# Performance work log

Measured on AMD Instinct MI355X. Metric: run time of the kernel, lower is better.

Reference implementation:

```python
import jax, jax.numpy as jnp
import numpy as np

NEG_SLOPE = 0.2


def gat_conv(x, src, dst, W, a_src, a_dst, bias, concat):
    # x: [N, F_in]; W: [F_in, H*C]; a_src/a_dst: [H, C]
    n = x.shape[0]
    H, C = a_src.shape
    h = (x @ W).reshape(n, H, C)                      # [N, H, C]
    alpha_s = jnp.einsum('nhc,hc->nh', h, a_src)       # [N, H]
    alpha_d = jnp.einsum('nhc,hc->nh', h, a_dst)
    e = alpha_s[src] + alpha_d[dst]                    # [E, H]
    e = jax.nn.leaky_relu(e, NEG_SLOPE)
    # scatter-softmax over incoming edges of each dst node
    m = jax.ops.segment_max(e, dst, num_segments=n)    # [N, H]
    ex = jnp.exp(e - m[dst])                           # [E, H]
    s = jax.ops.segment_sum(ex, dst, num_segments=n)   # [N, H]
    alpha = ex / (s[dst] + 1e-16)                      # [E, H]
    # weighted scatter-sum aggregation
    out = jax.ops.segment_sum(alpha[:, :, None] * h[src], dst, num_segments=n)  # [N, H, C]
    out = out.reshape(n, H * C) if concat else out.mean(axis=1)
    return out + bias


def setup_inputs() -> dict:
    key = jax.random.key(0)
    ks = jax.random.split(key, 10)
    N, E, F_IN, HID, H0 = 50000, 800000, 128, 64, 4
    sc = 0.1
    return {
        'x': jax.random.normal(ks[0], (N, F_IN), dtype=jnp.float32),
        'edge_index': jax.random.randint(ks[1], (2, E), 0, N, dtype=jnp.int32),
        'W0': jax.random.normal(ks[2], (F_IN, H0 * HID), dtype=jnp.float32) * sc,
        'att_src0': jax.random.normal(ks[3], (H0, HID), dtype=jnp.float32) * sc,
        'att_dst0': jax.random.normal(ks[4], (H0, HID), dtype=jnp.float32) * sc,
        'bias0': jax.random.normal(ks[5], (H0 * HID,), dtype=jnp.float32) * sc,
        'W1': jax.random.normal(ks[6], (H0 * HID, HID), dtype=jnp.float32) * sc,
        'att_src1': jax.random.normal(ks[7], (1, HID), dtype=jnp.float32) * sc,
        'att_dst1': jax.random.normal(ks[8], (1, HID), dtype=jnp.float32) * sc,
        'bias1': jax.random.normal(ks[9], (HID,), dtype=jnp.float32) * sc,
    }


def reference(x, edge_index, W0, att_src0, att_dst0, bias0, W1, att_src1, att_dst1, bias1):
    n = x.shape[0]
    loop = jnp.arange(n, dtype=edge_index.dtype)
    src = jnp.concatenate([edge_index[0], loop])  # PyG GATConv add_self_loops=True
    dst = jnp.concatenate([edge_index[1], loop])
    h = gat_conv(x, src, dst, W0, att_src0, att_dst0, bias0, concat=True)   # [N, 256]
    h = jax.nn.elu(h)  # activation between layers (ELU)
    out = gat_conv(h, src, dst, W1, att_src1, att_dst1, bias1, concat=False)  # [N, 64]
    return out
```

## Files before the change

### kernel.cpp

```cpp
#include <hip/hip_runtime.h>
#include <hip/hip_fp16.h>

#define NEG_SLOPE 0.2f
#define SLOTS 64
#define WSHIFT 4.0f

typedef _Float16 half8 __attribute__((ext_vector_type(8)));
typedef float f32x4 __attribute__((ext_vector_type(4)));

__device__ __forceinline__ float lrelu(float x) { return x > 0.f ? x : NEG_SLOPE * x; }
__device__ __forceinline__ float elu(float x) { return x > 0.f ? x : (__expf(x) - 1.f); }

__global__ void scatter_kernel(const int* __restrict__ src, const int* __restrict__ dst,
                               int E, int* __restrict__ cnt, unsigned short* __restrict__ slots) {
    int stride = gridDim.x * blockDim.x;
    for (int i = blockIdx.x * blockDim.x + threadIdx.x; i < E; i += stride) {
        int d = dst[i];
        int slot = atomicAdd(&cnt[d], 1);
        if (slot < SLOTS) slots[(size_t)d * SLOTS + slot] = (unsigned short)src[i];
    }
}

__global__ __launch_bounds__(256) void prep_kernel(
        const float* __restrict__ W0, const float* __restrict__ W1,
        const float* __restrict__ a_s, const float* __restrict__ a_d,
        float* __restrict__ Wa, __half* __restrict__ Wt0, __half* __restrict__ Wt1) {
    int t = blockIdx.x * 256 + threadIdx.x;
    if (t < 512) {
        int k = t >> 2, h = t & 3;
        float ss = 0.f, dd = 0.f;
        for (int c = 0; c < 64; c++) {
            float w = W0[(size_t)k * 256 + h * 64 + c];
            ss += w * a_s[h * 64 + c];
            dd += w * a_d[h * 64 + c];
        }
        Wa[k * 8 + h] = ss;
        Wa[k * 8 + 4 + h] = dd;
    } else if (t < 512 + 256 * 128) {
        int i = t - 512;
        int c = i >> 7, k = i & 127;
        Wt0[i] = __float2half_rn(W0[(size_t)k * 256 + c]);
    } else if (t < 512 + 256 * 128 + 64 * 256) {
        int i = t - 512 - 256 * 128;
        int c = i >> 8, k = i & 255;
        Wt1[i] = __float2half_rn(W1[(size_t)k * 64 + c]);
    }
}

__global__ __launch_bounds__(256) void gemv0_kernel(const float* __restrict__ x, const float* __restrict__ Wa,
                                                    int N, __half* __restrict__ xh,
                                                    float* __restrict__ as0, float* __restrict__ ad0) {
    int wid = (blockIdx.x * 256 + threadIdx.x) >> 6;
    int lane = threadIdx.x & 63;
    if (wid >= N) return;
    float2 xv = *(const float2*)(x + (size_t)wid * 128 + lane * 2);
    *(__half2*)(xh + (size_t)wid * 128 + lane * 2) = __floats2half2_rn(xv.x, xv.y);
    float p[8];
#pragma unroll
    for (int j = 0; j < 8; j++)
        p[j] = xv.x * Wa[(lane * 2) * 8 + j] + xv.y * Wa[(lane * 2 + 1) * 8 + j];
#pragma unroll
    for (int off = 32; off; off >>= 1)
#pragma unroll
        for (int j = 0; j < 8; j++) p[j] += __shfl_xor(p[j], off);
    if (lane == 0) {
        *(float4*)(as0 + (size_t)wid * 4) = make_float4(p[0], p[1], p[2], p[3]);
        *(float4*)(ad0 + (size_t)wid * 4) = make_float4(p[4], p[5], p[6], p[7]);
    }
}

__global__ __launch_bounds__(256) void agg0_kernel(
        const int* __restrict__ cnt, const unsigned short* __restrict__ slots,
        const float* __restrict__ as0, const float* __restrict__ ad0,
        const __half* __restrict__ xh, int N, __half* __restrict__ aggx) {
    int wid = (blockIdx.x * 256 + threadIdx.x) >> 6;
    int lane = threadIdx.x & 63;
    if (wid >= N) return;
    int deg = min(cnt[wid], SLOTS - 1);
    int degT = deg + 1;
    const int g = lane >> 4, lg = lane & 15;
    float4 adv = *(const float4*)(ad0 + (size_t)wid * 4);

    int s_l = 0;
    unsigned wpx = 0, wpy = 0;
    float wsum[4] = {0.f, 0.f, 0.f, 0.f};
    if (lane < degT) {
        s_l = (lane < deg) ? (int)slots[(size_t)wid * SLOTS + lane] : wid;
        float4 asv = *(const float4*)(as0 + (size_t)s_l * 4);
        float w0 = __expf(lrelu(asv.x + adv.x) - WSHIFT);
        float w1 = __expf(lrelu(asv.y + adv.y) - WSHIFT);
        float w2 = __expf(lrelu(asv.z + adv.z) - WSHIFT);
        float w3 = __expf(lrelu(asv.w + adv.w) - WSHIFT);
        wsum[0] = w0; wsum[1] = w1; wsum[2] = w2; wsum[3] = w3;
        __half2 p01 = __floats2half2_rn(w0, w1);
        __half2 p23 = __floats2half2_rn(w2, w3);
        wpx = *(unsigned*)&p01;
        wpy = *(unsigned*)&p23;
    }

    __half2 acc2[4][4] = {};
    int kmax = (degT + 3) >> 2;
#pragma unroll 4
    for (int k = 0; k < kmax; k++) {
        int j = g + k * 4;
        int s = __shfl(s_l, j);
        unsigned ux = (unsigned)__shfl((int)wpx, j);
        unsigned uy = (unsigned)__shfl((int)wpy, j);
        half8 xv = *(const half8*)(xh + (size_t)s * 128 + lg * 8);
        __half2 p01 = *(__half2*)&ux;
        __half2 p23 = *(__half2*)&uy;
        __half2 w0 = __halves2half2(__low2half(p01), __low2half(p01));
        __half2 w1 = __halves2half2(__high2half(p01), __high2half(p01));
        __half2 w2 = __halves2half2(__low2half(p23), __low2half(p23));
        __half2 w3 = __halves2half2(__high2half(p23), __high2half(p23));
        const __half2* xv2 = (const __half2*)&xv;
#pragma unroll
        for (int c = 0; c < 4; c++) {
            acc2[0][c] = __hfma2(w0, xv2[c], acc2[0][c]);
            acc2[1][c] = __hfma2(w1, xv2[c], acc2[1][c]);
            acc2[2][c] = __hfma2(w2, xv2[c], acc2[2][c]);
            acc2[3][c] = __hfma2(w3, xv2[c], acc2[3][c]);
        }
    }

#pragma unroll
    for (int off = 16; off < 64; off <<= 1)
#pragma unroll
        for (int h = 0; h < 4; h++)
#pragma unroll
            for (int c = 0; c < 4; c++) {
                int raw = __shfl_xor(*(int*)&acc2[h][c], off);
                acc2[h][c] = __hadd2(acc2[h][c], *(__half2*)&raw);
            }
#pragma unroll
    for (int off = 32; off; off >>= 1)
#pragma unroll
        for (int h = 0; h < 4; h++) wsum[h] += __shfl_xor(wsum[h], off);

    if (g == 0) {
#pragma unroll
        for (int h = 0; h < 4; h++) {
            float iv = 1.f / (wsum[h] + 1e-16f);
            __half2 o[4];
#pragma unroll
            for (int c = 0; c < 4; c++) {
                float2 f = __half22float2(acc2[h][c]);
                o[c] = __floats2half2_rn(f.x * iv, f.y * iv);
            }
            *(uint4*)(aggx + ((size_t)h * N + wid) * 128 + lg * 8) = *(uint4*)o;
        }
    }
}

__global__ __launch_bounds__(256) void gemmA_kernel(
        const __half* __restrict__ aggx, const __half* __restrict__ Wt0,
        const float* __restrict__ bias0, int N, __half* __restrict__ h1) {
    __shared__ __half As[64][136];
    __shared__ __half Bs[64][136];
    const int head = blockIdx.y;
    const int block_row = blockIdx.x * 64;
    const int t = threadIdx.x;
    const __half* A = aggx + (size_t)head * N * 128;

#pragma unroll
    for (int ii = 0; ii < 4; ii++) {
        int i = t + ii * 256;
        int r = i >> 4, c4 = i & 15;
        int gr = block_row + r;
        uint4 av = make_uint4(0, 0, 0, 0);
        if (gr < N) av = *(const uint4*)(A + (size_t)gr * 128 + c4 * 8);
        *(uint4*)&As[r][c4 * 8] = av;
        *(uint4*)&Bs[r][c4 * 8] = *(const uint4*)(Wt0 + ((size_t)head * 64 + r) * 128 + c4 * 8);
    }
    __syncthreads();

    const int w = t >> 6, l15 = t & 15, l4 = (t & 63) >> 4;
    f32x4 acc[4];
#pragma unroll
    for (int ct = 0; ct < 4; ct++) acc[ct] = (f32x4){0.f, 0.f, 0.f, 0.f};
#pragma unroll
    for (int kk = 0; kk < 4; kk++) {
        half8 a = *(const half8*)&As[w * 16 + l15][kk * 32 + l4 * 8];
#pragma unroll
        for (int ct = 0; ct < 4; ct++) {
            half8 b = *(const half8*)&Bs[ct * 16 + l15][kk * 32 + l4 * 8];
            acc[ct] = __builtin_amdgcn_mfma_f32_16x16x32_f16(a, b, acc[ct], 0, 0, 0);
        }
    }
#pragma unroll
    for (int ct = 0; ct < 4; ct++) {
        int col = head * 64 + ct * 16 + l15;
        float bv = bias0[col];
#pragma unroll
        for (int reg = 0; reg < 4; reg++) {
            int row = block_row + w * 16 + l4 * 4 + reg;
            if (row < N) h1[(size_t)row * 256 + col] = __float2half_rn(elu(acc[ct][reg] + bv));
        }
    }
}

__global__ __launch_bounds__(256) void gemmB_kernel(
        const __half* __restrict__ h1, const __half* __restrict__ Wt1,
        const float* __restrict__ a_s, const float* __restrict__ a_d,
        int N, __half* __restrict__ h2, float* __restrict__ as1, float* __restrict__ ad1) {
    __shared__ __half As[64][136];
    __shared__ __half Bs[64][136];
    const int block_row = blockIdx.x * 64;
    const int t = threadIdx.x;
    const int w = t >> 6, l15 = t & 15, l4 = (t & 63) >> 4;
    f32x4 acc[4];
#pragma unroll
    for (int ct = 0; ct < 4; ct++) acc[ct] = (f32x4){0.f, 0.f, 0.f, 0.f};

    for (int kc = 0; kc < 2; kc++) {
        __syncthreads();
#pragma unroll
        for (int ii = 0; ii < 4; ii++) {
            int i = t + ii * 256;
            int r = i >> 4, c4 = i & 15;
            int gr = block_row + r;
            uint4 av = make_uint4(0, 0, 0, 0);
            if (gr < N) av = *(const uint4*)(h1 + (size_t)gr * 256 + kc * 128 + c4 * 8);
            *(uint4*)&As[r][c4 * 8] = av;
            *(uint4*)&Bs[r][c4 * 8] = *(const uint4*)(Wt1 + (size_t)r * 256 + kc * 128 + c4 * 8);
        }
        __syncthreads();
#pragma unroll
        for (int kk = 0; kk < 4; kk++) {
            half8 a = *(const half8*)&As[w * 16 + l15][kk * 32 + l4 * 8];
#pragma unroll
            for (int ct = 0; ct < 4; ct++) {
                half8 b = *(const half8*)&Bs[ct * 16 + l15][kk * 32 + l4 * 8];
                acc[ct] = __builtin_amdgcn_mfma_f32_16x16x32_f16(a, b, acc[ct], 0, 0, 0);
            }
        }
    }

    float asv[4], adv[4];
#pragma unroll
    for (int ct = 0; ct < 4; ct++) { asv[ct] = a_s[ct * 16 + l15]; adv[ct] = a_d[ct * 16 + l15]; }
#pragma unroll
    for (int reg = 0; reg < 4; reg++) {
        float sd = 0.f, dd = 0.f;
#pragma unroll
        for (int ct = 0; ct < 4; ct++) { sd += acc[ct][reg] * asv[ct]; dd += acc[ct][reg] * adv[ct]; }
#pragma unroll
        for (int off = 1; off < 16; off <<= 1) { sd += __shfl_xor(sd, off); dd += __shfl_xor(dd, off); }
        int row = block_row + w * 16 + l4 * 4 + reg;
        if (row < N) {
#pragma unroll
            for (int ct = 0; ct < 4; ct++)
                h2[(size_t)row * 64 + ct * 16 + l15] = __float2half_rn(acc[ct][reg]);
            if (l15 == 0) { as1[row] = sd; ad1[row] = dd; }
        }
    }
}

__global__ __launch_bounds__(256) void agg1_kernel(
        const int* __restrict__ cnt, const unsigned short* __restrict__ slots,
        const float* __restrict__ as1, const float* __restrict__ ad1,
        const __half* __restrict__ h2, const float* __restrict__ bias1,
        int N, float* __restrict__ out) {
    int wid = (blockIdx.x * 256 + threadIdx.x) >> 6;
    int lane = threadIdx.x & 63;
    if (wid >= N) return;
    int deg = min(cnt[wid], SLOTS - 1);
    int degT = deg + 1;
    const int g = lane >> 3, lg = lane & 7;
    float adv = ad1[wid];

    int s_l = 0;
    float w_l = 0.f;
    if (lane < degT) {
        s_l = (lane < deg) ? (int)slots[(size_t)wid * SLOTS + lane] : wid;
        w_l = __expf(lrelu(as1[s_l] + adv) - WSHIFT);
    }
    float wsum = w_l;

    __half2 acc2[4] = {};
    int kmax = (degT + 7) >> 3;
#pragma unroll 4
    for (int k = 0; k < kmax; k++) {
        int j = g + k * 8;
        int s = __shfl(s_l, j);
        float w = __shfl(w_l, j);
        __half hw = __float2half(w);
        __half2 ww = __halves2half2(hw, hw);
        half8 xv = *(const half8*)(h2 + (size_t)s * 64 + lg * 8);
        const __half2* xv2 = (const __half2*)&xv;
#pragma unroll
        for (int c = 0; c < 4; c++) acc2[c] = __hfma2(ww, xv2[c], acc2[c]);
    }
#pragma unroll
    for (int off = 8; off < 64; off <<= 1)
#pragma unroll
        for (int c = 0; c < 4; c++) {
            int raw = __shfl_xor(*(int*)&acc2[c], off);
            acc2[c] = __hadd2(acc2[c], *(__half2*)&raw);
        }
#pragma unroll
    for (int off = 32; off; off >>= 1) wsum += __shfl_xor(wsum, off);

    float iv = 1.f / (wsum + 1e-16f);
    if (g == 0) {
        float o[8];
#pragma unroll
        for (int c = 0; c < 4; c++) {
            float2 f = __half22float2(acc2[c]);
            o[2 * c]     = f.x * iv + bias1[lg * 8 + 2 * c];
            o[2 * c + 1] = f.y * iv + bias1[lg * 8 + 2 * c + 1];
        }
        *(float4*)(out + (size_t)wid * 64 + lg * 8)     = make_float4(o[0], o[1], o[2], o[3]);
        *(float4*)(out + (size_t)wid * 64 + lg * 8 + 4) = make_float4(o[4], o[5], o[6], o[7]);
    }
}

extern "C" void kernel_launch(void* const* d_in, const int* in_sizes, int n_in,
                              void* d_out, int out_size, void* d_ws, size_t ws_size,
                              hipStream_t stream) {
    const float* x    = (const float*)d_in[0];
    const int*   ei   = (const int*)d_in[1];
    const float* W0   = (const float*)d_in[2];
    const float* as0w = (const float*)d_in[3];
    const float* ad0w = (const float*)d_in[4];
    const float* b0   = (const float*)d_in[5];
    const float* W1   = (const float*)d_in[6];
    const float* as1w = (const float*)d_in[7];
    const float* ad1w = (const float*)d_in[8];
    const float* b1   = (const float*)d_in[9];
    float* out = (float*)d_out;

    const int HID = in_sizes[9];
    const int N   = out_size / HID;
    const int E   = in_sizes[1] / 2;
    const int* src = ei;
    const int* dst = ei + E;

    char* ws = (char*)d_ws;
    size_t off = 0;
    auto alloc = [&](size_t bytes) -> void* {
        off = (off + 255) & ~(size_t)255;
        void* p = ws + off;
        off += bytes;
        return p;
    };
    int*            cnt   = (int*)alloc((size_t)N * 4);
    unsigned short* slots = (unsigned short*)alloc((size_t)N * SLOTS * 2);
    float*  Wa       = (float*)alloc(128 * 8 * 4);
    __half* Wt0      = (__half*)alloc(256 * 128 * 2);
    __half* Wt1      = (__half*)alloc(64 * 256 * 2);
    float*  as0      = (float*)alloc((size_t)N * 4 * 4);
    float*  ad0v     = (float*)alloc((size_t)N * 4 * 4);
    __half* xh       = (__half*)alloc((size_t)N * 128 * 2);
    __half* aggx     = (__half*)alloc((size_t)N * 512 * 2);
    __half* h1       = (__half*)alloc((size_t)N * 256 * 2);
    __half* h2       = xh;
    float*  as1      = as0;
    float*  ad1v     = ad0v;

    hipMemsetAsync(cnt, 0, (size_t)N * 4, stream);
    prep_kernel<<<194, 256, 0, stream>>>(W0, W1, as0w, ad0w, Wa, Wt0, Wt1);
    gemv0_kernel<<<(N * 64 + 255) / 256, 256, 0, stream>>>(x, Wa, N, xh, as0, ad0v);
    scatter_kernel<<<2048, 256, 0, stream>>>(src, dst, E, cnt, slots);

    agg0_kernel<<<(N * 64 + 255) / 256, 256, 0, stream>>>(cnt, slots, as0, ad0v, xh, N, aggx);
    dim3 gA((N + 63) / 64, 4);
    gemmA_kernel<<<gA, 256, 0, stream>>>(aggx, Wt0, b0, N, h1);
    gemmB_kernel<<<(N + 63) / 64, 256, 0, stream>>>(h1, Wt1, as1w, ad1w, N, h2, as1, ad1v);
    agg1_kernel<<<(N * 64 + 255) / 256, 256, 0, stream>>>(cnt, slots, as1, ad1v, h2, b1, N, out);
}
```

Baseline: 192.4 us.

## Fuse layer-0 head GEMMs with layer-1 GEMM, keeping h1 in shared memory

Merges the per-head layer-0 projection GEMM (bias+ELU) and the layer-1 projection GEMM into one kernel. Each block computes all four heads for its 64 rows into a shared-memory h1 tile, then runs the second GEMM from that tile, so the N×256 half-precision h1 round trip through global memory and one launch are gone. Weight operands are now read straight from global memory (likely cache hits) rather than staged in LDS. In exchange, the grid is a quarter the size, the heads run serially per block, and the larger LDS footprint may reduce occupancy.

```diff
diff --git a/kernel.cpp b/kernel.cpp
--- a/kernel.cpp
+++ b/kernel.cpp
@@ -152,86 +152,68 @@
     }
 }
 
-__global__ __launch_bounds__(256) void gemmA_kernel(
+__global__ __launch_bounds__(256) void gemmAB_kernel(
         const __half* __restrict__ aggx, const __half* __restrict__ Wt0,
-        const float* __restrict__ bias0, int N, __half* __restrict__ h1) {
-    __shared__ __half As[64][136];
-    __shared__ __half Bs[64][136];
-    const int head = blockIdx.y;
-    const int block_row = blockIdx.x * 64;
-    const int t = threadIdx.x;
-    const __half* A = aggx + (size_t)head * N * 128;
-
-#pragma unroll
-    for (int ii = 0; ii < 4; ii++) {
-        int i = t + ii * 256;
-        int r = i >> 4, c4 = i & 15;
-        int gr = block_row + r;
-        uint4 av = make_uint4(0, 0, 0, 0);
-        if (gr < N) av = *(const uint4*)(A + (size_t)gr * 128 + c4 * 8);
-        *(uint4*)&As[r][c4 * 8] = av;
-        *(uint4*)&Bs[r][c4 * 8] = *(const uint4*)(Wt0 + ((size_t)head * 64 + r) * 128 + c4 * 8);
-    }
-    __syncthreads();
-
-    const int w = t >> 6, l15 = t & 15, l4 = (t & 63) >> 4;
-    f32x4 acc[4];
-#pragma unroll
-    for (int ct = 0; ct < 4; ct++) acc[ct] = (f32x4){0.f, 0.f, 0.f, 0.f};
-#pragma unroll
-    for (int kk = 0; kk < 4; kk++) {
-        half8 a = *(const half8*)&As[w * 16 + l15][kk * 32 + l4 * 8];
-#pragma unroll
-        for (int ct = 0; ct < 4; ct++) {
-            half8 b = *(const half8*)&Bs[ct * 16 + l15][kk * 32 + l4 * 8];
-            acc[ct] = __builtin_amdgcn_mfma_f32_16x16x32_f16(a, b, acc[ct], 0, 0, 0);
-        }
-    }
-#pragma unroll
-    for (int ct = 0; ct < 4; ct++) {
-        int col = head * 64 + ct * 16 + l15;
-        float bv = bias0[col];
-#pragma unroll
-        for (int reg = 0; reg < 4; reg++) {
-            int row = block_row + w * 16 + l4 * 4 + reg;
-            if (row < N) h1[(size_t)row * 256 + col] = __float2half_rn(elu(acc[ct][reg] + bv));
-        }
-    }
-}
-
-__global__ __launch_bounds__(256) void gemmB_kernel(
-        const __half* __restrict__ h1, const __half* __restrict__ Wt1,
+        const __half* __restrict__ Wt1, const float* __restrict__ bias0,
         const float* __restrict__ a_s, const float* __restrict__ a_d,
         int N, __half* __restrict__ h2, float* __restrict__ as1, float* __restrict__ ad1) {
     __shared__ __half As[64][136];
-    __shared__ __half Bs[64][136];
+    __shared__ __half h1s[64][264];
     const int block_row = blockIdx.x * 64;
     const int t = threadIdx.x;
     const int w = t >> 6, l15 = t & 15, l4 = (t & 63) >> 4;
-    f32x4 acc[4];
-#pragma unroll
-    for (int ct = 0; ct < 4; ct++) acc[ct] = (f32x4){0.f, 0.f, 0.f, 0.f};
-
-    for (int kc = 0; kc < 2; kc++) {
+
+    for (int head = 0; head < 4; head++) {
         __syncthreads();
+        const __half* A = aggx + (size_t)head * N * 128;
 #pragma unroll
         for (int ii = 0; ii < 4; ii++) {
             int i = t + ii * 256;
             int r = i >> 4, c4 = i & 15;
             int gr = block_row + r;
             uint4 av = make_uint4(0, 0, 0, 0);
-            if (gr < N) av = *(const uint4*)(h1 + (size_t)gr * 256 + kc * 128 + c4 * 8);
+            if (gr < N) av = *(const uint4*)(A + (size_t)gr * 128 + c4 * 8);
             *(uint4*)&As[r][c4 * 8] = av;
-            *(uint4*)&Bs[r][c4 * 8] = *(const uint4*)(Wt1 + (size_t)r * 256 + kc * 128 + c4 * 8);
         }
         __syncthreads();
+
+        f32x4 acc[4];
+#pragma unroll
+        for (int ct = 0; ct < 4; ct++) acc[ct] = (f32x4){0.f, 0.f, 0.f, 0.f};
 #pragma unroll
         for (int kk = 0; kk < 4; kk++) {
             half8 a = *(const half8*)&As[w * 16 + l15][kk * 32 + l4 * 8];
 #pragma unroll
             for (int ct = 0; ct < 4; ct++) {
-                half8 b = *(const half8*)&Bs[ct * 16 + l15][kk * 32 + l4 * 8];
+                half8 b = *(const half8*)(Wt0 + ((size_t)head * 64 + ct * 16 + l15) * 128 + kk * 32 + l4 * 8);
                 acc[ct] = __builtin_amdgcn_mfma_f32_16x16x32_f16(a, b, acc[ct], 0, 0, 0);
+            }
+        }
+#pragma unroll
+        for (int ct = 0; ct < 4; ct++) {
+            int col = head * 64 + ct * 16 + l15;
+            float bv = bias0[col];
+#pragma unroll
+            for (int reg = 0; reg < 4; reg++) {
+                int rloc = w * 16 + l4 * 4 + reg;
+                h1s[rloc][col] = __float2half_rn(elu(acc[ct][reg] + bv));
+            }
+        }
+    }
+    __syncthreads();
+
+    f32x4 acc2[4];
+#pragma unroll
+    for (int ct = 0; ct < 4; ct++) acc2[ct] = (f32x4){0.f, 0.f, 0.f, 0.f};
+#pragma unroll
+    for (int kc = 0; kc < 2; kc++) {
+#pragma unroll
+        for (int kk = 0; kk < 4; kk++) {
+            half8 a = *(const half8*)&h1s[w * 16 + l15][kc * 128 + kk * 32 + l4 * 8];
+#pragma unroll
+            for (int ct = 0; ct < 4; ct++) {
+                half8 b = *(const half8*)(Wt1 + (size_t)(ct * 16 + l15) * 256 + kc * 128 + kk * 32 + l4 * 8);
+                acc2[ct] = __builtin_amdgcn_mfma_f32_16x16x32_f16(a, b, acc2[ct], 0, 0, 0);
             }
         }
     }
@@ -243,14 +225,14 @@
     for (int reg = 0; reg < 4; reg++) {
         float sd = 0.f, dd = 0.f;
 #pragma unroll
-        for (int ct = 0; ct < 4; ct++) { sd += acc[ct][reg] * asv[ct]; dd += acc[ct][reg] * adv[ct]; }
+        for (int ct = 0; ct < 4; ct++) { sd += acc2[ct][reg] * asv[ct]; dd += acc2[ct][reg] * adv[ct]; }
 #pragma unroll
         for (int off = 1; off < 16; off <<= 1) { sd += __shfl_xor(sd, off); dd += __shfl_xor(dd, off); }
         int row = block_row + w * 16 + l4 * 4 + reg;
         if (row < N) {
 #pragma unroll
             for (int ct = 0; ct < 4; ct++)
-                h2[(size_t)row * 64 + ct * 16 + l15] = __float2half_rn(acc[ct][reg]);
+                h2[(size_t)row * 64 + ct * 16 + l15] = __float2half_rn(acc2[ct][reg]);
             if (l15 == 0) { as1[row] = sd; ad1[row] = dd; }
         }
     }
@@ -353,7 +335,6 @@
     float*  ad0v     = (float*)alloc((size_t)N * 4 * 4);
     __half* xh       = (__half*)alloc((size_t)N * 128 * 2);
     __half* aggx     = (__half*)alloc((size_t)N * 512 * 2);
-    __half* h1       = (__half*)alloc((size_t)N * 256 * 2);
     __half* h2       = xh;
     float*  as1      = as0;
     float*  ad1v     = ad0v;
@@ -364,8 +345,6 @@
     scatter_kernel<<<2048, 256, 0, stream>>>(src, dst, E, cnt, slots);
 
     agg0_kernel<<<(N * 64 + 255) / 256, 256, 0, stream>>>(cnt, slots, as0, ad0v, xh, N, aggx);
-    dim3 gA((N + 63) / 64, 4);
-    gemmA_kernel<<<gA, 256, 0, stream>>>(aggx, Wt0, b0, N, h1);
-    gemmB_kernel<<<(N + 63) / 64, 256, 0, stream>>>(h1, Wt1, as1w, ad1w, N, h2, as1, ad1v);
+    gemmAB_kernel<<<(N + 63) / 64, 256, 0, stream>>>(aggx, Wt0, Wt1, b0, as1w, ad1w, N, h2, as1, ad1v);
     agg1_kernel<<<(N * 64 + 255) / 256, 256, 0, stream>>>(cnt, slots, as1, ad1v, h2, b1, N, out);
 }
```

Result: slower. 214.7 us (+11.6%).
